# Kernel optimization log

Hardware: AMD Instinct MI355X
Metric: run time of the kernel (lower is better)

Reference implementation:

```python
import jax, jax.numpy as jnp
import numpy as np

D_MODEL = 1024
NUM_HEADS = 16
D_K = D_MODEL // NUM_HEADS


def setup_inputs() -> dict:
    key = jax.random.key(0)
    k1, k2, k3, kq, kk, kv, ko = jax.random.split(key, 7)
    B, S = 4, 2048
    scale = 1.0 / np.sqrt(D_MODEL)
    return {
        "Q_in": jax.random.normal(k1, (B, S, D_MODEL), dtype=jnp.float32),
        "K_in": jax.random.normal(k2, (B, S, D_MODEL), dtype=jnp.float32),
        "V_in": jax.random.normal(k3, (B, S, D_MODEL), dtype=jnp.float32),
        "W_q": jax.random.normal(kq, (D_MODEL, D_MODEL), dtype=jnp.float32) * scale,
        "W_k": jax.random.normal(kk, (D_MODEL, D_MODEL), dtype=jnp.float32) * scale,
        "W_v": jax.random.normal(kv, (D_MODEL, D_MODEL), dtype=jnp.float32) * scale,
        "W_o": jax.random.normal(ko, (D_MODEL, D_MODEL), dtype=jnp.float32) * scale,
    }


def _split_heads(x):
    B, S, _ = x.shape
    return x.reshape(B, S, NUM_HEADS, D_K).transpose(0, 2, 1, 3)  # [B,H,S,d_k]


def reference(Q_in, K_in, V_in, W_q, W_k, W_v, W_o):
    # nn.Linear: y = x @ W.T ; here W_* stored as [out, in] equivalent square,
    # use x @ W.T convention to match torch.
    Q = _split_heads(Q_in @ W_q.T)
    K = _split_heads(K_in @ W_k.T)
    V = _split_heads(V_in @ W_v.T)
    scores = jnp.einsum("bhqd,bhkd->bhqk", Q, K) / jnp.sqrt(jnp.float32(D_K))
    attn = jax.nn.softmax(scores, axis=-1)  # [B,H,S,S]
    out = jnp.einsum("bhqk,bhkd->bhqd", attn, V)
    B, H, S, dk = out.shape
    concat = out.transpose(0, 2, 1, 3).reshape(B, S, H * dk)
    return concat @ W_o.T
```

## Files before the change

kernel.cpp:

```cpp
#include <hip/hip_runtime.h>
#include <math.h>

typedef __bf16 bf16x8v __attribute__((ext_vector_type(8)));
typedef float f32x4 __attribute__((ext_vector_type(4)));
typedef float f32x16 __attribute__((ext_vector_type(16)));

__device__ __forceinline__ void async_copy16(void* lds, const void* g) {
  __builtin_amdgcn_global_load_lds(
      (const __attribute__((address_space(1))) void*)g,
      (__attribute__((address_space(3))) void*)lds, 16, 0, 0);
}

struct CastArgs {
  const float* s[7];
  __bf16* d[7];
};
__global__ __launch_bounds__(256) void cast_kernel(CastArgs a) {
  const int t = blockIdx.y;
  const int n = (t < 3) ? 8388608 : 1048576;
  const int i = (blockIdx.x * 256 + threadIdx.x) * 8;
  if (i >= n) return;
  const float4 v0 = *(const float4*)(a.s[t] + i);
  const float4 v1 = *(const float4*)(a.s[t] + i + 4);
  bf16x8v o;
  o[0] = (__bf16)v0.x; o[1] = (__bf16)v0.y; o[2] = (__bf16)v0.z; o[3] = (__bf16)v0.w;
  o[4] = (__bf16)v1.x; o[5] = (__bf16)v1.y; o[6] = (__bf16)v1.z; o[7] = (__bf16)v1.w;
  *(bf16x8v*)(a.d[t] + i) = o;
}

template <int MODE, typename OutT>
__global__ __launch_bounds__(512) void gemm_bt(const __bf16* A, const __bf16* B,
                                               OutT* C,
                                               const __bf16* A2, const __bf16* B2,
                                               OutT* C2,
                                               int M, int N, int K) {
  __shared__ __bf16 As0[128 * 64];
  __shared__ __bf16 Bs0[128 * 64];
  __shared__ __bf16 As1[128 * 64];
  __shared__ __bf16 Bs1[128 * 64];
  if (blockIdx.z == 1) { A = A2; B = B2; C = C2; }
  const int tid = threadIdx.x;
  const int wave = tid >> 6, lane = tid & 63;
  const int lgrp = lane >> 4, lmod = lane & 15;
  const int bm = (MODE == 3 ? blockIdx.y : blockIdx.x) * 128;
  const int bn = (MODE == 3 ? blockIdx.x : blockIdx.y) * 128;
  const int wm = (wave >> 2) * 64, wn = (wave & 3) * 32;

  const __bf16* aSrc[2];
  const __bf16* bSrc[2];
  int slot[2];
#pragma unroll
  for (int i = 0; i < 2; i++) {
    const int s = i * 512 + tid;
    const int r = s >> 3, cb = s & 7;
    const int gc = (cb ^ (r & 7)) * 8;
    slot[i] = s * 8;
    aSrc[i] = A + (size_t)(bm + r) * K + gc;
    bSrc[i] = B + (size_t)(bn + r) * K + gc;
  }

  f32x4 acc[4][2];
#pragma unroll
  for (int mi = 0; mi < 4; mi++)
#pragma unroll
    for (int ni = 0; ni < 2; ni++)
#pragma unroll
      for (int r = 0; r < 4; r++) acc[mi][ni][r] = 0.f;

  auto STAGE = [&](int c, __bf16* Ad, __bf16* Bd) {
#pragma unroll
    for (int i = 0; i < 2; i++) {
      async_copy16(&Ad[slot[i]], aSrc[i] + (size_t)c * 64);
      async_copy16(&Bd[slot[i]], bSrc[i] + (size_t)c * 64);
    }
  };

  auto COMPUTE = [&](const __bf16* Abuf, const __bf16* Bbuf) {
#pragma unroll
    for (int ks = 0; ks < 2; ks++) {
      bf16x8v af[4], bf[2];
#pragma unroll
      for (int mi = 0; mi < 4; mi++) {
        const int row = wm + mi * 16 + lmod;
        af[mi] = *(const bf16x8v*)&Abuf[row * 64 + ((ks * 4 + lgrp) ^ (row & 7)) * 8];
      }
#pragma unroll
      for (int ni = 0; ni < 2; ni++) {
        const int row = wn + ni * 16 + lmod;
        bf[ni] = *(const bf16x8v*)&Bbuf[row * 64 + ((ks * 4 + lgrp) ^ (row & 7)) * 8];
      }
#pragma unroll
      for (int mi = 0; mi < 4; mi++)
#pragma unroll
        for (int ni = 0; ni < 2; ni++)
          acc[mi][ni] = __builtin_amdgcn_mfma_f32_16x16x32_bf16(af[mi], bf[ni],
                                                                acc[mi][ni], 0, 0, 0);
    }
  };

  STAGE(0, As0, Bs0);
  __syncthreads();
#pragma unroll 1
  for (int t = 0; t < 7; t++) {
    STAGE(2 * t + 1, As1, Bs1);
    COMPUTE(As0, Bs0);
    __syncthreads();
    STAGE(2 * t + 2, As0, Bs0);
    COMPUTE(As1, Bs1);
    __syncthreads();
  }
  STAGE(15, As1, Bs1);
  COMPUTE(As0, Bs0);
  __syncthreads();
  COMPUTE(As1, Bs1);

#pragma unroll
  for (int mi = 0; mi < 4; mi++)
#pragma unroll
    for (int ni = 0; ni < 2; ni++)
#pragma unroll
      for (int r = 0; r < 4; r++) {
        const int row = bm + wm + mi * 16 + lgrp * 4 + r;
        const int col = bn + wn + ni * 16 + lmod;
        if (MODE == 0) {
          C[(size_t)row * N + col] = (OutT)acc[mi][ni][r];
        } else if (MODE == 1) {
          C[(size_t)(row >> 11) * 2097152 + (size_t)(col >> 6) * 131072 +
            (size_t)(row & 2047) * 64 + (col & 63)] = (OutT)acc[mi][ni][r];
        } else {
          C[(size_t)(col >> 11) * 2097152 + (size_t)(row >> 6) * 131072 +
            (size_t)(row & 63) * 2048 + (col & 2047)] = (OutT)acc[mi][ni][r];
        }
      }
}

__global__ __launch_bounds__(256) void attn_kernel(const __bf16* __restrict__ Qh,
                                                   const __bf16* __restrict__ Kh,
                                                   const __bf16* __restrict__ Vt,
                                                   __bf16* __restrict__ O) {
  __shared__ __bf16 Ks0[64 * 64];
  __shared__ __bf16 Ks1[64 * 64];
  __shared__ __bf16 Vts0[64 * 64];
  __shared__ __bf16 Vts1[64 * 64];

  const int tid = threadIdx.x;
  const int wave = tid >> 6, lane = tid & 63;
  const int l31 = lane & 31, hi = lane >> 5;
  const int qt = blockIdx.y, y = blockIdx.x;
  const size_t hb = (size_t)y * 131072;
  const __bf16* Qb = Qh + hb + (size_t)qt * 128 * 64;
  const __bf16* Kb = Kh + hb;
  const __bf16* Vb = Vt + hb;
  const int wq0 = wave * 32;

  const int s0 = tid, s1 = 256 + tid;
  const int kr0 = s0 >> 3, kc0 = s0 & 7;
  const int kr1 = s1 >> 3, kc1 = s1 & 7;
  const __bf16* kSrc0 = Kb + (size_t)kr0 * 64 + (kc0 ^ (kr0 & 7)) * 8;
  const __bf16* kSrc1 = Kb + (size_t)kr1 * 64 + (kc1 ^ (kr1 & 7)) * 8;
  const __bf16* vSrc0 = Vb + (size_t)kr0 * 2048 + (kc0 ^ (kr0 & 7)) * 8;
  const __bf16* vSrc1 = Vb + (size_t)kr1 * 2048 + (kc1 ^ (kr1 & 7)) * 8;

  const float qscale = 0.125f * 1.44269504f;
  bf16x8v qf[4];
#pragma unroll
  for (int ks = 0; ks < 4; ks++) {
    bf16x8v q = *(const bf16x8v*)&Qb[(wq0 + l31) * 64 + ks * 16 + hi * 8];
#pragma unroll
    for (int j = 0; j < 8; j++) q[j] = (__bf16)((float)q[j] * qscale);
    qf[ks] = q;
  }

  float m_run = -INFINITY;
  float l_run = 0.f;
  f32x16 oacc[2];
#pragma unroll
  for (int nd = 0; nd < 2; nd++)
#pragma unroll
    for (int r = 0; r < 16; r++) oacc[nd][r] = 0.f;

  auto STAGE = [&](int c, __bf16* Kd, __bf16* Vd) {
    async_copy16(&Kd[s0 * 8], kSrc0 + (size_t)c * 4096);
    async_copy16(&Kd[s1 * 8], kSrc1 + (size_t)c * 4096);
    async_copy16(&Vd[s0 * 8], vSrc0 + (size_t)c * 64);
    async_copy16(&Vd[s1 * 8], vSrc1 + (size_t)c * 64);
  };

  auto COMPUTE = [&](const __bf16* Kbuf, const __bf16* Vbuf) {
    f32x16 st[2];
#pragma unroll
    for (int kvt = 0; kvt < 2; kvt++)
#pragma unroll
      for (int r = 0; r < 16; r++) st[kvt][r] = 0.f;
#pragma unroll
    for (int ks = 0; ks < 4; ks++) {
      const int sl = ((ks * 2 + hi) ^ (l31 & 7)) * 8;
      const bf16x8v kf0 = *(const bf16x8v*)&Kbuf[l31 * 64 + sl];
      const bf16x8v kf1 = *(const bf16x8v*)&Kbuf[(32 + l31) * 64 + sl];
      __builtin_amdgcn_s_setprio(1);
      st[0] = __builtin_amdgcn_mfma_f32_32x32x16_bf16(kf0, qf[ks], st[0], 0, 0, 0);
      st[1] = __builtin_amdgcn_mfma_f32_32x32x16_bf16(kf1, qf[ks], st[1], 0, 0, 0);
      __builtin_amdgcn_s_setprio(0);
    }

    float bmax[16];
#pragma unroll
    for (int j = 0; j < 16; j++) bmax[j] = fmaxf(st[0][j], st[1][j]);
#pragma unroll
    for (int s = 8; s > 0; s >>= 1)
#pragma unroll
      for (int j = 0; j < 8; j++)
        if (j < s) bmax[j] = fmaxf(bmax[j], bmax[j + s]);
    float rmax = bmax[0];
    rmax = fmaxf(rmax, __shfl_xor(rmax, 32));

    if (!__all(rmax - m_run <= 8.f)) {
      const float mnew = fmaxf(m_run, rmax);
      const float alpha = __builtin_amdgcn_exp2f(m_run - mnew);
      m_run = mnew;
      l_run *= alpha;
#pragma unroll
      for (int r = 0; r < 16; r++) {
        const float ar = __shfl(alpha, (r & 3) + 8 * (r >> 2) + 4 * hi);
        oacc[0][r] *= ar;
        oacc[1][r] *= ar;
      }
    }

    float psum = 0.f;
#pragma unroll
    for (int kvt = 0; kvt < 2; kvt++) {
#pragma unroll
      for (int sub = 0; sub < 2; sub++) {
        const int ks2 = kvt * 2 + sub;
        const int vs = ((ks2 * 2 + hi) ^ (l31 & 7)) * 8;
        const bf16x8v vf0 = *(const bf16x8v*)&Vbuf[l31 * 64 + vs];
        const bf16x8v vf1 = *(const bf16x8v*)&Vbuf[(32 + l31) * 64 + vs];
        const int o = sub * 8;
        float p[8];
#pragma unroll
        for (int j = 0; j < 8; j++) {
          p[j] = __builtin_amdgcn_exp2f(st[kvt][o + j] - m_run);
          psum += p[j];
        }
        unsigned x0, y0, x1, y1;
        asm("v_cvt_pk_bf16_f32 %0, %1, %2" : "=v"(x0) : "v"(p[0]), "v"(p[1]));
        asm("v_cvt_pk_bf16_f32 %0, %1, %2" : "=v"(y0) : "v"(p[4]), "v"(p[5]));
        asm("v_cvt_pk_bf16_f32 %0, %1, %2" : "=v"(x1) : "v"(p[2]), "v"(p[3]));
        asm("v_cvt_pk_bf16_f32 %0, %1, %2" : "=v"(y1) : "v"(p[6]), "v"(p[7]));
        asm("v_permlane32_swap_b32 %0, %1" : "+v"(x0), "+v"(y0));
        asm("v_permlane32_swap_b32 %0, %1" : "+v"(x1), "+v"(y1));
        union { unsigned u[4]; bf16x8v v; } af;
        af.u[0] = x0; af.u[1] = x1; af.u[2] = y0; af.u[3] = y1;
        __builtin_amdgcn_s_setprio(1);
        oacc[0] = __builtin_amdgcn_mfma_f32_32x32x16_bf16(af.v, vf0, oacc[0], 0, 0, 0);
        oacc[1] = __builtin_amdgcn_mfma_f32_32x32x16_bf16(af.v, vf1, oacc[1], 0, 0, 0);
        __builtin_amdgcn_s_setprio(0);
      }
    }
    l_run += psum;
  };

  STAGE(0, Ks0, Vts0);
  __syncthreads();
#pragma unroll 1
  for (int t = 0; t < 15; t++) {
    STAGE(2 * t + 1, Ks1, Vts1);
    COMPUTE(Ks0, Vts0);
    __syncthreads();
    STAGE(2 * t + 2, Ks0, Vts0);
    COMPUTE(Ks1, Vts1);
    __syncthreads();
  }
  STAGE(31, Ks1, Vts1);
  COMPUTE(Ks0, Vts0);
  __syncthreads();
  COMPUTE(Ks1, Vts1);

  l_run += __shfl_xor(l_run, 32);
  const float linv = 1.f / l_run;
  const int b = y >> 4, h = y & 15;
#pragma unroll
  for (int r = 0; r < 16; r++) {
    const int q = (r & 3) + 8 * (r >> 2) + 4 * hi;
    const float inv = __shfl(linv, q);
    const int srow = qt * 128 + wq0 + q;
    const size_t base = ((size_t)(b * 2048 + srow)) * 1024 + h * 64;
    O[base + l31] = (__bf16)(oacc[0][r] * inv);
    O[base + 32 + l31] = (__bf16)(oacc[1][r] * inv);
  }
}

extern "C" void kernel_launch(void* const* d_in, const int* in_sizes, int n_in,
                              void* d_out, int out_size, void* d_ws, size_t ws_size,
                              hipStream_t stream) {
  const float* Qin = (const float*)d_in[0];
  const float* Kin = (const float*)d_in[1];
  const float* Vin = (const float*)d_in[2];
  const float* Wq = (const float*)d_in[3];
  const float* Wk = (const float*)d_in[4];
  const float* Wv = (const float*)d_in[5];
  const float* Wo = (const float*)d_in[6];
  float* out = (float*)d_out;

  __bf16* base = (__bf16*)d_ws;
  __bf16* Qbf = base;
  __bf16* Kbf = base + 8388608;
  __bf16* Vbf = base + 16777216;
  __bf16* Wqb = base + 25165824;
  __bf16* Wkb = base + 26214400;
  __bf16* Wvb = base + 27262976;
  __bf16* Wob = base + 28311552;
  __bf16* Qh = base + 29360128;
  __bf16* Kh = base + 37748736;
  __bf16* Vt = base + 46137344;
  __bf16* AO = Qbf;

  CastArgs ca;
  ca.s[0] = Qin; ca.s[1] = Kin; ca.s[2] = Vin;
  ca.s[3] = Wq;  ca.s[4] = Wk;  ca.s[5] = Wv;  ca.s[6] = Wo;
  ca.d[0] = Qbf; ca.d[1] = Kbf; ca.d[2] = Vbf;
  ca.d[3] = Wqb; ca.d[4] = Wkb; ca.d[5] = Wvb; ca.d[6] = Wob;
  cast_kernel<<<dim3(4096, 7), 256, 0, stream>>>(ca);

  const int M = 8192, N = 1024, K = 1024;
  dim3 bb(512);
  gemm_bt<1, __bf16><<<dim3(64, 8, 2), bb, 0, stream>>>(Qbf, Wqb, Qh,
                                                        Kbf, Wkb, Kh, M, N, K);
  gemm_bt<3, __bf16><<<dim3(64, 8), bb, 0, stream>>>(Wvb, Vbf, Vt,
                                                     nullptr, nullptr, nullptr,
                                                     1024, 8192, K);
  attn_kernel<<<dim3(64, 16), dim3(256), 0, stream>>>(Qh, Kh, Vt, AO);
  gemm_bt<0, float><<<dim3(64, 8), bb, 0, stream>>>(AO, Wob, out,
                                                    nullptr, nullptr, nullptr,
                                                    M, N, K);
}
```

Before: 320.5 us.

## Merge V projection into batched QK GEMM launch and tighten softmax reductions

The V projection (transposed output layout) now runs as a third z-slice of the batched Q/K projection GEMM launch, so one kernel launch and its tail are removed and all three projections share one grid. In the attention kernel, the row-max reduction uses v_max3_f32 trees instead of pairwise fmax, and the probability sum uses packed v_pk_add_f32 to cut VALU instruction count. The merged launch assumes M=N swapped dimensions line up for the V slice, with M/N/K passed as the Q/K values, which happens to match here since K is shared and the swapped bm/bn handles the transpose.

```diff
diff --git a/kernel.cpp b/kernel.cpp
--- a/kernel.cpp
+++ b/kernel.cpp
@@ -2,6 +2,7 @@
 #include <math.h>
 
 typedef __bf16 bf16x8v __attribute__((ext_vector_type(8)));
+typedef float f32x2 __attribute__((ext_vector_type(2)));
 typedef float f32x4 __attribute__((ext_vector_type(4)));
 typedef float f32x16 __attribute__((ext_vector_type(16)));
 
@@ -9,6 +10,17 @@
   __builtin_amdgcn_global_load_lds(
       (const __attribute__((address_space(1))) void*)g,
       (__attribute__((address_space(3))) void*)lds, 16, 0, 0);
+}
+
+__device__ __forceinline__ f32x2 pk_add(f32x2 a, f32x2 b) {
+  f32x2 d;
+  asm("v_pk_add_f32 %0, %1, %2" : "=v"(d) : "v"(a), "v"(b));
+  return d;
+}
+__device__ __forceinline__ float max3f(float a, float b, float c) {
+  float d;
+  asm("v_max3_f32 %0, %1, %2, %3" : "=v"(d) : "v"(a), "v"(b), "v"(c));
+  return d;
 }
 
 struct CastArgs {
@@ -33,17 +45,23 @@
                                                OutT* C,
                                                const __bf16* A2, const __bf16* B2,
                                                OutT* C2,
+                                               const __bf16* A3, const __bf16* B3,
+                                               OutT* C3,
                                                int M, int N, int K) {
   __shared__ __bf16 As0[128 * 64];
   __shared__ __bf16 Bs0[128 * 64];
   __shared__ __bf16 As1[128 * 64];
   __shared__ __bf16 Bs1[128 * 64];
-  if (blockIdx.z == 1) { A = A2; B = B2; C = C2; }
+  const bool vz = (MODE == 1 && blockIdx.z == 2);
+  if (MODE == 1) {
+    if (blockIdx.z == 1) { A = A2; B = B2; C = C2; }
+    else if (blockIdx.z == 2) { A = A3; B = B3; C = C3; }
+  }
   const int tid = threadIdx.x;
   const int wave = tid >> 6, lane = tid & 63;
   const int lgrp = lane >> 4, lmod = lane & 15;
-  const int bm = (MODE == 3 ? blockIdx.y : blockIdx.x) * 128;
-  const int bn = (MODE == 3 ? blockIdx.x : blockIdx.y) * 128;
+  const int bm = ((MODE == 3 || vz) ? blockIdx.y : blockIdx.x) * 128;
+  const int bn = ((MODE == 3 || vz) ? blockIdx.x : blockIdx.y) * 128;
   const int wm = (wave >> 2) * 64, wn = (wave & 3) * 32;
 
   const __bf16* aSrc[2];
@@ -124,7 +142,7 @@
         const int col = bn + wn + ni * 16 + lmod;
         if (MODE == 0) {
           C[(size_t)row * N + col] = (OutT)acc[mi][ni][r];
-        } else if (MODE == 1) {
+        } else if (MODE == 1 && !vz) {
           C[(size_t)(row >> 11) * 2097152 + (size_t)(col >> 6) * 131072 +
             (size_t)(row & 2047) * 64 + (col & 63)] = (OutT)acc[mi][ni][r];
         } else {
@@ -203,15 +221,18 @@
       __builtin_amdgcn_s_setprio(0);
     }
 
-    float bmax[16];
-#pragma unroll
-    for (int j = 0; j < 16; j++) bmax[j] = fmaxf(st[0][j], st[1][j]);
-#pragma unroll
-    for (int s = 8; s > 0; s >>= 1)
-#pragma unroll
-      for (int j = 0; j < 8; j++)
-        if (j < s) bmax[j] = fmaxf(bmax[j], bmax[j + s]);
-    float rmax = bmax[0];
+    float w[11];
+#pragma unroll
+    for (int g = 0; g < 10; g++) {
+      const int i0 = 3 * g, i1 = 3 * g + 1, i2 = 3 * g + 2;
+      w[g] = max3f(st[i0 >> 4][i0 & 15], st[i1 >> 4][i1 & 15], st[i2 >> 4][i2 & 15]);
+    }
+    w[10] = fmaxf(st[1][14], st[1][15]);
+    const float x0 = max3f(w[0], w[1], w[2]);
+    const float x1 = max3f(w[3], w[4], w[5]);
+    const float x2 = max3f(w[6], w[7], w[8]);
+    const float x3 = fmaxf(w[9], w[10]);
+    float rmax = fmaxf(max3f(x0, x1, x2), x3);
     rmax = fmaxf(rmax, __shfl_xor(rmax, 32));
 
     if (!__all(rmax - m_run <= 8.f)) {
@@ -227,7 +248,8 @@
       }
     }
 
-    float psum = 0.f;
+    f32x2 lsum;
+    lsum[0] = 0.f; lsum[1] = 0.f;
 #pragma unroll
     for (int kvt = 0; kvt < 2; kvt++) {
 #pragma unroll
@@ -239,10 +261,12 @@
         const int o = sub * 8;
         float p[8];
 #pragma unroll
-        for (int j = 0; j < 8; j++) {
+        for (int j = 0; j < 8; j++)
           p[j] = __builtin_amdgcn_exp2f(st[kvt][o + j] - m_run);
-          psum += p[j];
-        }
+        f32x2 a, b, c, d;
+        a[0] = p[0]; a[1] = p[1]; b[0] = p[2]; b[1] = p[3];
+        c[0] = p[4]; c[1] = p[5]; d[0] = p[6]; d[1] = p[7];
+        lsum = pk_add(lsum, pk_add(pk_add(a, b), pk_add(c, d)));
         unsigned x0, y0, x1, y1;
         asm("v_cvt_pk_bf16_f32 %0, %1, %2" : "=v"(x0) : "v"(p[0]), "v"(p[1]));
         asm("v_cvt_pk_bf16_f32 %0, %1, %2" : "=v"(y0) : "v"(p[4]), "v"(p[5]));
@@ -258,7 +282,7 @@
         __builtin_amdgcn_s_setprio(0);
       }
     }
-    l_run += psum;
+    l_run += lsum[0] + lsum[1];
   };
 
   STAGE(0, Ks0, Vts0);
@@ -325,13 +349,10 @@
 
   const int M = 8192, N = 1024, K = 1024;
   dim3 bb(512);
-  gemm_bt<1, __bf16><<<dim3(64, 8, 2), bb, 0, stream>>>(Qbf, Wqb, Qh,
-                                                        Kbf, Wkb, Kh, M, N, K);
-  gemm_bt<3, __bf16><<<dim3(64, 8), bb, 0, stream>>>(Wvb, Vbf, Vt,
-                                                     nullptr, nullptr, nullptr,
-                                                     1024, 8192, K);
+  gemm_bt<1, __bf16><<<dim3(64, 8, 3), bb, 0, stream>>>(
+      Qbf, Wqb, Qh, Kbf, Wkb, Kh, Wvb, Vbf, Vt, M, N, K);
   attn_kernel<<<dim3(64, 16), dim3(256), 0, stream>>>(Qh, Kh, Vt, AO);
-  gemm_bt<0, float><<<dim3(64, 8), bb, 0, stream>>>(AO, Wob, out,
-                                                    nullptr, nullptr, nullptr,
-                                                    M, N, K);
-}
+  gemm_bt<0, float><<<dim3(64, 8), bb, 0, stream>>>(
+      AO, Wob, out, nullptr, nullptr, nullptr, nullptr, nullptr, nullptr,
+      M, N, K);
+}
```

Result: no change. 318.8 us (-0.5%).
